# Kernel optimization log

Hardware: AMD Instinct MI355X
Metric: run time of the kernel (lower is better)

## Reference

```python
import jax, jax.numpy as jnp
import numpy as np

N, H = 16, 200
EMB, H1, H2 = 64, 128, 64
NUM_SKILLS = 2000
D_USER, D_ITEM, D_LANG = 100, 100, 10
TIME_BINS = np.array([1, 3600, 24 * 3600, 7 * 24 * 3600], dtype=np.float32)
NUM_TIME_CATS = TIME_BINS.size + 2  # 6

# strictly-lower-triangular pair indices, row-major: pair (i, j) with j < i
PAIR_I, PAIR_J = np.tril_indices(H, k=-1)          # skill_indices, history_indices_selected
P = PAIR_I.size                                    # adjusted_history_len = H*(H-1)/2
ar = np.arange(H)
SUM_IDX = np.concatenate([ar * (ar - 1) // 2, [H * (H - 1) // 2]]).astype(np.int64)  # len H+1


def setup_inputs() -> dict:
    key = jax.random.key(0)
    ks = jax.random.split(key, 16)
    users = jax.random.normal(ks[0], (N, D_USER), jnp.float32)
    items = jax.random.normal(ks[1], (N * H, D_ITEM), jnp.float32)
    langs = jax.random.normal(ks[2], (N * H, D_LANG), jnp.float32)
    skills = jax.random.randint(ks[3], (N, H), 0, NUM_SKILLS)
    timestamps = jnp.sort(jax.random.uniform(ks[4], (N, H), jnp.float32) * 2e6, axis=1)
    targets = (jax.random.uniform(ks[5], (N, H)) > 0.5).astype(jnp.float32)
    mask = jnp.ones((N * H,), dtype=bool)
    emb_table = jax.random.normal(ks[6], (NUM_SKILLS, EMB), jnp.float32) * 0.1
    emb_table = emb_table.at[0].set(0.0)  # padding_idx=0
    W1 = jax.random.normal(ks[7], (H1, 2 * EMB + NUM_TIME_CATS), jnp.float32) * 0.05
    b1 = jnp.zeros((H1,), jnp.float32)
    W2 = jax.random.normal(ks[8], (H2, H1), jnp.float32) * 0.05
    b2 = jnp.zeros((H2,), jnp.float32)
    W3 = jax.random.normal(ks[9], (1, H2), jnp.float32) * 0.05
    b3 = jnp.zeros((1,), jnp.float32)
    num_features = D_USER + D_ITEM + D_LANG + NUM_SKILLS
    linW = jax.random.normal(ks[10], (1, num_features + 2 * NUM_SKILLS), jnp.float32) * 0.01
    linb = jnp.zeros((1,), jnp.float32)
    return {"users": users, "items": items, "langs": langs, "skills": skills,
            "timestamps": timestamps, "targets": targets, "mask": mask,
            "emb_table": emb_table, "W1": W1, "b1": b1, "W2": W2, "b2": b2,
            "W3": W3, "b3": b3, "linW": linW, "linb": linb}


def _forward(users, items, langs, skills, timestamps, targets, mask,
             emb_table, W1, b1, W2, b2, W3, b3, linW, linb):
    bins = jnp.asarray(TIME_BINS)
    pi = jnp.asarray(PAIR_I)
    pj = jnp.asarray(PAIR_J)
    # gather pair embeddings: [N*P, EMB]
    emb = emb_table[skills]                       # [N, H, EMB]
    e_i = emb[:, pi].reshape(-1, EMB)             # skill at position i
    e_j = emb[:, pj].reshape(-1, EMB)             # history skill j < i
    # time-delta categories
    dt = (timestamps[:, pi] - timestamps[:, pj]).reshape(-1)
    cats = jnp.sum(dt[:, None] > bins[None, :], axis=1) + 1
    pad = skills == 0
    pad_pair = pad[:, pi].reshape(-1) | pad[:, pj].reshape(-1)
    cats = jnp.where(pad_pair, 0, cats)
    dt_oh = jax.nn.one_hot(cats, NUM_TIME_CATS, dtype=jnp.float32)
    # pairwise similarity MLP -> tanh scalar, [N, P]
    x = jnp.concatenate([e_i, e_j, dt_oh], axis=1)
    h = jax.nn.relu(x @ W1.T + b1)
    h = jax.nn.relu(h @ W2.T + b2)
    sim = jnp.tanh(h @ W3.T + b3).reshape(N, P)

    sum_idx = jnp.asarray(SUM_IDX)

    def seg_sum(v):  # cumsum-based segment sum over pairs grouped by i -> [N, H]
        cs = jnp.concatenate([jnp.zeros((N, 1), v.dtype), jnp.cumsum(v, axis=1)], axis=1)
        return cs[:, sum_idx[1:]] - cs[:, sum_idx[:-1]]

    flat_skills = skills.reshape(-1)              # [N*H]
    padf = (flat_skills != 0).astype(jnp.float32)
    rows = jnp.arange(N * H)
    v_total = seg_sum(sim).reshape(-1) * padf
    v_correct = seg_sum(sim * targets[:, pi]).reshape(-1) * padf
    tcf = jnp.zeros((N * H, 2 * NUM_SKILLS), jnp.float32)
    tcf = tcf.at[rows, flat_skills].set(v_total)
    tcf = tcf.at[rows, flat_skills + NUM_SKILLS].set(v_correct)

    feats = jnp.concatenate([
        jnp.repeat(users, H, axis=0), items, langs,
        jax.nn.one_hot(flat_skills, NUM_SKILLS, dtype=jnp.float32), tcf], axis=1)
    logits = feats @ linW.T + linb                # [N*H, 1]
    preds = logits.reshape(-1)
    labels = targets.reshape(-1)
    maskf = mask.astype(jnp.float32)
    # BCEWithLogits (reduction='none') + z-term, z_weight=0.0; mask applied as weight
    bce = jnp.logaddexp(0.0, preds) - preds * labels
    eps = 1e-6
    yc = jnp.clip(labels, eps, 1.0 - eps)
    z = jnp.log(yc / (1.0 - yc))
    z_weight = 0.0
    loss = (bce + z_weight * jnp.square(z - preds)) * maskf
    return loss, jax.nn.sigmoid(preds), labels


def reference(users, items, langs, skills, timestamps, targets, mask,
              emb_table, W1, b1, W2, b2, W3, b3, linW, linb):
    return _forward(users, items, langs, skills, timestamps, targets, mask,
                    emb_table, W1, b1, W2, b2, W3, b3, linW, linb)
```

## Files before the change

### kernel.cpp

```cpp
#include <hip/hip_runtime.h>
#include <math.h>

#define N_B     16
#define H_LEN   200
#define NH      3200
#define P_PAIRS 19900
#define NP_TOT  318400
#define EMB     64
#define HID1    128
#define HID2    64
#define NCAT    6
#define W1_COLS 134

#define WS_A    0
#define WS_B    409600
#define WS_C    819200
#define WS_VT   819968
#define WS_W2   823168
#define WS_W1T  827264

#define TI 16
#define NTILE_I 13
#define NTRI (NTILE_I * (NTILE_I + 1) / 2)

typedef __attribute__((ext_vector_type(8))) __bf16 bf16x8;
typedef __attribute__((ext_vector_type(8))) short short8;
typedef __attribute__((ext_vector_type(4))) float f32x4;

__global__ void k0_setup(const float* __restrict__ W1,
                         const float* __restrict__ b1,
                         const float* __restrict__ W2,
                         float* __restrict__ ws) {
    int idx = blockIdx.x * 256 + threadIdx.x;
    if (idx < 17152) {
        int c = idx >> 7, t = idx & 127;
        ws[WS_W1T + c * 128 + t] = W1[t * W1_COLS + c];
        return;
    }
    idx -= 17152;
    if (idx < HID2 * HID1) {
        __bf16 h = (__bf16)W2[idx];
        ((unsigned short*)(ws + WS_W2))[idx] = __builtin_bit_cast(unsigned short, h);
        return;
    }
    idx -= HID2 * HID1;
    if (idx < NCAT * HID1) {
        int c = idx >> 7, t = idx & 127;
        ws[WS_C + idx] = W1[t * W1_COLS + 2 * EMB + c] + b1[t];
        return;
    }
    idx -= NCAT * HID1;
    if (idx < NH) ws[WS_VT + idx] = 0.f;
}

__global__ __launch_bounds__(256)
void k1_ab(const int* __restrict__ skills,
           const float* __restrict__ emb,
           float* __restrict__ ws) {
    __shared__ float e[16][68];
    int t = threadIdx.x;
    int r0 = blockIdx.x * 16;
    {
        int r = t >> 4, c = t & 15;
        int s = skills[r0 + r];
        float4 x = *(const float4*)(emb + (size_t)s * EMB + c * 4);
        *(float4*)&e[r][c * 4] = x;
    }
    __syncthreads();
    int half = t >> 7;
    int c = t & 127;
    const float* w1t = ws + WS_W1T + half * EMB * 128;
    float acc[16];
    #pragma unroll
    for (int r = 0; r < 16; ++r) acc[r] = 0.f;
    #pragma unroll 4
    for (int k0 = 0; k0 < EMB; k0 += 4) {
        float wv0 = w1t[(k0 + 0) * 128 + c];
        float wv1 = w1t[(k0 + 1) * 128 + c];
        float wv2 = w1t[(k0 + 2) * 128 + c];
        float wv3 = w1t[(k0 + 3) * 128 + c];
        #pragma unroll
        for (int r = 0; r < 16; ++r) {
            float4 ev = *(const float4*)&e[r][k0];
            acc[r] = fmaf(wv0, ev.x, acc[r]);
            acc[r] = fmaf(wv1, ev.y, acc[r]);
            acc[r] = fmaf(wv2, ev.z, acc[r]);
            acc[r] = fmaf(wv3, ev.w, acc[r]);
        }
    }
    size_t outbase = half ? WS_B : WS_A;
    #pragma unroll
    for (int r = 0; r < 16; ++r)
        ws[outbase + (size_t)(r0 + r) * HID1 + c] = acc[r];
}

__global__ __launch_bounds__(256, 2)
void k2_mfma(const int* __restrict__ skills,
             const float* __restrict__ ts,
             const float* __restrict__ b2,
             const float* __restrict__ W3,
             const float* __restrict__ b3,
             float* __restrict__ ws) {
    __shared__ float Asm[TI][132];
    __shared__ float Bsm[TI][132];
    __shared__ float Csm[NCAT][132];
    __shared__ float tsi[TI], tsj[TI];
    __shared__ int   ski[TI], skj[TI];

    int t = threadIdx.x, lane = t & 63, w = t >> 6;
    int col = lane & 15, quad = lane >> 4;

    int bid = blockIdx.x;
    int n = bid & 15;
    int tt = bid >> 4;
    int ti = (int)((sqrtf(8.f * (float)tt + 1.f) - 1.f) * 0.5f);
    while (ti * (ti + 1) / 2 > tt) --ti;
    while ((ti + 1) * (ti + 2) / 2 <= tt) ++ti;
    int tj = tt - ti * (ti + 1) / 2;
    int i0 = ti * TI, j0 = tj * TI;
    int base = n * H_LEN;
    bool diag = (ti == tj);

    const short8* w2p = (const short8*)(ws + WS_W2);
    short8 afr[4][4];
    #pragma unroll
    for (int mt = 0; mt < 4; ++mt)
        #pragma unroll
        for (int kk = 0; kk < 4; ++kk)
            afr[mt][kk] = w2p[(mt * 16 + col) * 16 + kk * 4 + quad];
    float b2v[16], w3v[16];
    #pragma unroll
    for (int mt = 0; mt < 4; ++mt)
        #pragma unroll
        for (int r = 0; r < 4; ++r) {
            int u = mt * 16 + quad * 4 + r;
            b2v[mt * 4 + r] = b2[u];
            w3v[mt * 4 + r] = W3[u];
        }
    float b3s = b3[0];

    {
        int r = t >> 5, c = t & 31;
        int gi = min(i0 + r, H_LEN - 1);
        int gi2 = min(i0 + r + 8, H_LEN - 1);
        *(float4*)&Asm[r][c * 4]     = *(const float4*)(ws + WS_A + (size_t)(base + gi)  * HID1 + c * 4);
        *(float4*)&Asm[r + 8][c * 4] = *(const float4*)(ws + WS_A + (size_t)(base + gi2) * HID1 + c * 4);
        int gj = min(j0 + r, H_LEN - 1);
        int gj2 = min(j0 + r + 8, H_LEN - 1);
        *(float4*)&Bsm[r][c * 4]     = *(const float4*)(ws + WS_B + (size_t)(base + gj)  * HID1 + c * 4);
        *(float4*)&Bsm[r + 8][c * 4] = *(const float4*)(ws + WS_B + (size_t)(base + gj2) * HID1 + c * 4);
        if (t < NCAT * 32) {
            int cr = t >> 5, cc = t & 31;
            *(float4*)&Csm[cr][cc * 4] = *(const float4*)(ws + WS_C + cr * HID1 + cc * 4);
        }
        if (t < TI) {
            int gii = min(i0 + t, H_LEN - 1);
            int gjj = min(j0 + t, H_LEN - 1);
            tsi[t] = ts[base + gii]; ski[t] = skills[base + gii];
            tsj[t] = ts[base + gjj]; skj[t] = skills[base + gjj];
        }
    }
    __syncthreads();

    #pragma unroll
    for (int s = 0; s < 4; ++s) {
        int ii = w * 4 + s;
        int gi = i0 + ii;
        if (gi >= H_LEN) continue;
        if (diag && ii == 0) continue;

        int si = ski[ii];  float tsiv = tsi[ii];
        int sj = skj[col]; float tsjv = tsj[col];
        float dtv = tsiv - tsjv;
        int cat = (si == 0 || sj == 0) ? 0
                : 1 + (dtv > 1.f) + (dtv > 3600.f) + (dtv > 86400.f) + (dtv > 604800.f);

        f32x4 acc[4] = {{0.f, 0.f, 0.f, 0.f}, {0.f, 0.f, 0.f, 0.f},
                        {0.f, 0.f, 0.f, 0.f}, {0.f, 0.f, 0.f, 0.f}};
        #pragma unroll
        for (int kk = 0; kk < 4; ++kk) {
            int d0 = kk * 32 + quad * 8;
            float4 a0 = *(const float4*)&Asm[ii][d0];
            float4 a1 = *(const float4*)&Asm[ii][d0 + 4];
            float4 bb0 = *(const float4*)&Bsm[col][d0];
            float4 bb1 = *(const float4*)&Bsm[col][d0 + 4];
            float4 c0 = *(const float4*)&Csm[cat][d0];
            float4 c1 = *(const float4*)&Csm[cat][d0 + 4];
            bf16x8 v;
            v[0] = (__bf16)fmaxf(a0.x + bb0.x + c0.x, 0.f);
            v[1] = (__bf16)fmaxf(a0.y + bb0.y + c0.y, 0.f);
            v[2] = (__bf16)fmaxf(a0.z + bb0.z + c0.z, 0.f);
            v[3] = (__bf16)fmaxf(a0.w + bb0.w + c0.w, 0.f);
            v[4] = (__bf16)fmaxf(a1.x + bb1.x + c1.x, 0.f);
            v[5] = (__bf16)fmaxf(a1.y + bb1.y + c1.y, 0.f);
            v[6] = (__bf16)fmaxf(a1.z + bb1.z + c1.z, 0.f);
            v[7] = (__bf16)fmaxf(a1.w + bb1.w + c1.w, 0.f);
            #pragma unroll
            for (int mt = 0; mt < 4; ++mt)
                acc[mt] = __builtin_amdgcn_mfma_f32_16x16x32_bf16(
                    __builtin_bit_cast(bf16x8, afr[mt][kk]), v, acc[mt], 0, 0, 0);
        }

        float partial = 0.f;
        #pragma unroll
        for (int mt = 0; mt < 4; ++mt)
            #pragma unroll
            for (int r = 0; r < 4; ++r) {
                float h2 = fmaxf(acc[mt][r] + b2v[mt * 4 + r], 0.f);
                partial = fmaf(h2, w3v[mt * 4 + r], partial);
            }
        partial += __shfl_xor(partial, 16);
        partial += __shfl_xor(partial, 32);
        float sim = tanhf(partial + b3s);

        int gj = j0 + col;
        bool valid = (gj < gi);
        sim = valid ? sim : 0.f;
        sim += __shfl_xor(sim, 1);
        sim += __shfl_xor(sim, 2);
        sim += __shfl_xor(sim, 4);
        sim += __shfl_xor(sim, 8);
        if (lane == 0) atomicAdd(&ws[WS_VT + base + gi], sim);
    }
}

__global__ __launch_bounds__(256)
void k3_final(const float* __restrict__ users,
              const float* __restrict__ items,
              const float* __restrict__ langs,
              const int* __restrict__ skills,
              const float* __restrict__ targets,
              const float* __restrict__ linW,
              const float* __restrict__ linb,
              const float* __restrict__ ws,
              float* __restrict__ out) {
    int r = blockIdx.x * 4 + (threadIdx.x >> 6);
    int lane = threadIdx.x & 63;
    int n = r / H_LEN;
    float acc = 0.f;
    for (int idx = lane; idx < 210; idx += 64) {
        float f;
        if (idx < 100)      f = users[n * 100 + idx];
        else if (idx < 200) f = items[r * 100 + (idx - 100)];
        else                f = langs[r * 10 + (idx - 200)];
        acc = fmaf(f, linW[idx], acc);
    }
    #pragma unroll
    for (int off = 32; off > 0; off >>= 1) acc += __shfl_xor(acc, off);
    if (lane == 0) {
        int s = skills[r];
        float tgt = targets[r];
        float vtv = ws[WS_VT + r];
        if (s == 0) vtv = 0.f;
        float vcv = vtv * tgt;
        float logit = acc + linW[210 + s] + vtv * linW[2210 + s]
                    + vcv * linW[4210 + s] + linb[0];
        float sp = logit > 0.f ? logit + log1pf(expf(-logit)) : log1pf(expf(logit));
        float loss = sp - logit * tgt;
        float sig = 1.f / (1.f + expf(-logit));
        out[r]          = loss;
        out[NH + r]     = sig;
        out[2 * NH + r] = tgt;
    }
}

extern "C" void kernel_launch(void* const* d_in, const int* in_sizes, int n_in,
                              void* d_out, int out_size, void* d_ws, size_t ws_size,
                              hipStream_t stream) {
    const float* users   = (const float*)d_in[0];
    const float* items   = (const float*)d_in[1];
    const float* langs   = (const float*)d_in[2];
    const int*   skills  = (const int*)d_in[3];
    const float* ts      = (const float*)d_in[4];
    const float* targets = (const float*)d_in[5];
    const float* emb     = (const float*)d_in[7];
    const float* W1      = (const float*)d_in[8];
    const float* b1      = (const float*)d_in[9];
    const float* W2      = (const float*)d_in[10];
    const float* b2      = (const float*)d_in[11];
    const float* W3      = (const float*)d_in[12];
    const float* b3      = (const float*)d_in[13];
    const float* linW    = (const float*)d_in[14];
    const float* linb    = (const float*)d_in[15];
    float* ws  = (float*)d_ws;
    float* out = (float*)d_out;

    hipLaunchKernelGGL(k0_setup, dim3(115), dim3(256), 0, stream, W1, b1, W2, ws);
    hipLaunchKernelGGL(k1_ab, dim3(NH / 16), dim3(256), 0, stream, skills, emb, ws);
    hipLaunchKernelGGL(k2_mfma, dim3(N_B * NTRI), dim3(256), 0, stream,
                       skills, ts, b2, W3, b3, ws);
    hipLaunchKernelGGL(k3_final, dim3(NH / 4), dim3(256), 0, stream,
                       users, items, langs, skills, targets, linW, linb, ws, out);
}
```

Measured before the change: 125.0 us.

## Store hidden-layer projections in bf16 and pre-swizzle W2 fragments

The per-row A/B projections and the category+bias table are now stored as bf16 instead of fp32. This halves workspace traffic and LDS footprint, and the first-layer sum is unpacked with bit shifts. W2 is pre-permuted into MFMA fragment order so each lane makes one coalesced load. The B row is hoisted out of the per-i loop, occupancy is raised to 3 waves via launch bounds, and tanhf is replaced with a clamped exp-based formula. The cost is extra rounding of the layer-1 partial sums to bf16 before the add and ReLU.

```diff
diff --git a/kernel.cpp b/kernel.cpp
--- a/kernel.cpp
+++ b/kernel.cpp
@@ -4,28 +4,41 @@
 #define N_B     16
 #define H_LEN   200
 #define NH      3200
-#define P_PAIRS 19900
-#define NP_TOT  318400
 #define EMB     64
 #define HID1    128
 #define HID2    64
 #define NCAT    6
 #define W1_COLS 134
 
-#define WS_A    0
-#define WS_B    409600
-#define WS_C    819200
-#define WS_VT   819968
-#define WS_W2   823168
-#define WS_W1T  827264
-
 #define TI 16
 #define NTILE_I 13
 #define NTRI (NTILE_I * (NTILE_I + 1) / 2)
 
+#define WS_VT   0
+#define WS_W2F  3200
+#define WS_CB   7296
+#define WS_W1T  7680
+#define WS_A    24832
+#define WS_B    229632
+
 typedef __attribute__((ext_vector_type(8))) __bf16 bf16x8;
-typedef __attribute__((ext_vector_type(8))) short short8;
+typedef __attribute__((ext_vector_type(8))) unsigned short ushort8;
 typedef __attribute__((ext_vector_type(4))) float f32x4;
+
+__device__ __forceinline__ unsigned short bfbits(float x) {
+    return __builtin_bit_cast(unsigned short, (__bf16)x);
+}
+__device__ __forceinline__ void h1two(unsigned a, unsigned b, unsigned c,
+                                      bf16x8& v, int p) {
+    float s0 = __builtin_bit_cast(float, a << 16)
+             + __builtin_bit_cast(float, b << 16)
+             + __builtin_bit_cast(float, c << 16);
+    float s1 = __builtin_bit_cast(float, a & 0xFFFF0000u)
+             + __builtin_bit_cast(float, b & 0xFFFF0000u)
+             + __builtin_bit_cast(float, c & 0xFFFF0000u);
+    v[p]     = (__bf16)fmaxf(s0, 0.f);
+    v[p + 1] = (__bf16)fmaxf(s1, 0.f);
+}
 
 __global__ void k0_setup(const float* __restrict__ W1,
                          const float* __restrict__ b1,
@@ -38,15 +51,17 @@
         return;
     }
     idx -= 17152;
-    if (idx < HID2 * HID1) {
-        __bf16 h = (__bf16)W2[idx];
-        ((unsigned short*)(ws + WS_W2))[idx] = __builtin_bit_cast(unsigned short, h);
+    if (idx < 8192) {
+        int e = idx & 7, lane = (idx >> 3) & 63, f = idx >> 9;
+        int mt = f >> 2, kk = f & 3, col = lane & 15, quad = lane >> 4;
+        float w = W2[(mt * 16 + col) * HID1 + (kk * 4 + quad) * 8 + e];
+        ((unsigned short*)(ws + WS_W2F))[idx] = bfbits(w);
         return;
     }
-    idx -= HID2 * HID1;
+    idx -= 8192;
     if (idx < NCAT * HID1) {
         int c = idx >> 7, t = idx & 127;
-        ws[WS_C + idx] = W1[t * W1_COLS + 2 * EMB + c] + b1[t];
+        ((unsigned short*)(ws + WS_CB))[idx] = bfbits(W1[t * W1_COLS + 2 * EMB + c] + b1[t]);
         return;
     }
     idx -= NCAT * HID1;
@@ -88,22 +103,22 @@
             acc[r] = fmaf(wv3, ev.w, acc[r]);
         }
     }
-    size_t outbase = half ? WS_B : WS_A;
+    unsigned short* dst = (unsigned short*)(ws + (half ? WS_B : WS_A));
     #pragma unroll
     for (int r = 0; r < 16; ++r)
-        ws[outbase + (size_t)(r0 + r) * HID1 + c] = acc[r];
-}
-
-__global__ __launch_bounds__(256, 2)
+        dst[(size_t)(r0 + r) * HID1 + c] = bfbits(acc[r]);
+}
+
+__global__ __launch_bounds__(256, 3)
 void k2_mfma(const int* __restrict__ skills,
              const float* __restrict__ ts,
              const float* __restrict__ b2,
              const float* __restrict__ W3,
              const float* __restrict__ b3,
              float* __restrict__ ws) {
-    __shared__ float Asm[TI][132];
-    __shared__ float Bsm[TI][132];
-    __shared__ float Csm[NCAT][132];
+    __shared__ unsigned short Asm[TI][136];
+    __shared__ unsigned short Bsm[TI][136];
+    __shared__ unsigned short Csm[NCAT][136];
     __shared__ float tsi[TI], tsj[TI];
     __shared__ int   ski[TI], skj[TI];
 
@@ -121,13 +136,13 @@
     int base = n * H_LEN;
     bool diag = (ti == tj);
 
-    const short8* w2p = (const short8*)(ws + WS_W2);
-    short8 afr[4][4];
+    const ushort8* w2f = (const ushort8*)(ws + WS_W2F);
+    bf16x8 afr[4][4];
     #pragma unroll
     for (int mt = 0; mt < 4; ++mt)
         #pragma unroll
         for (int kk = 0; kk < 4; ++kk)
-            afr[mt][kk] = w2p[(mt * 16 + col) * 16 + kk * 4 + quad];
+            afr[mt][kk] = __builtin_bit_cast(bf16x8, w2f[(mt * 4 + kk) * 64 + lane]);
     float b2v[16], w3v[16];
     #pragma unroll
     for (int mt = 0; mt < 4; ++mt)
@@ -140,18 +155,17 @@
     float b3s = b3[0];
 
     {
-        int r = t >> 5, c = t & 31;
+        int r = t >> 4, c = t & 15;
         int gi = min(i0 + r, H_LEN - 1);
-        int gi2 = min(i0 + r + 8, H_LEN - 1);
-        *(float4*)&Asm[r][c * 4]     = *(const float4*)(ws + WS_A + (size_t)(base + gi)  * HID1 + c * 4);
-        *(float4*)&Asm[r + 8][c * 4] = *(const float4*)(ws + WS_A + (size_t)(base + gi2) * HID1 + c * 4);
         int gj = min(j0 + r, H_LEN - 1);
-        int gj2 = min(j0 + r + 8, H_LEN - 1);
-        *(float4*)&Bsm[r][c * 4]     = *(const float4*)(ws + WS_B + (size_t)(base + gj)  * HID1 + c * 4);
-        *(float4*)&Bsm[r + 8][c * 4] = *(const float4*)(ws + WS_B + (size_t)(base + gj2) * HID1 + c * 4);
-        if (t < NCAT * 32) {
-            int cr = t >> 5, cc = t & 31;
-            *(float4*)&Csm[cr][cc * 4] = *(const float4*)(ws + WS_C + cr * HID1 + cc * 4);
+        const unsigned short* pA = (const unsigned short*)(ws + WS_A);
+        const unsigned short* pB = (const unsigned short*)(ws + WS_B);
+        *(ushort8*)&Asm[r][c * 8] = *(const ushort8*)(pA + (size_t)(base + gi) * HID1 + c * 8);
+        *(ushort8*)&Bsm[r][c * 8] = *(const ushort8*)(pB + (size_t)(base + gj) * HID1 + c * 8);
+        if (t < NCAT * 16) {
+            int cr = t >> 4, cc = t & 15;
+            *(ushort8*)&Csm[cr][cc * 8] =
+                *(const ushort8*)((const unsigned short*)(ws + WS_CB) + cr * HID1 + cc * 8);
         }
         if (t < TI) {
             int gii = min(i0 + t, H_LEN - 1);
@@ -162,6 +176,12 @@
     }
     __syncthreads();
 
+    uint4 braw[4];
+    #pragma unroll
+    for (int kk = 0; kk < 4; ++kk)
+        braw[kk] = *(const uint4*)&Bsm[col][kk * 32 + quad * 8];
+    int sj = skj[col]; float tsjv = tsj[col];
+
     #pragma unroll
     for (int s = 0; s < 4; ++s) {
         int ii = w * 4 + s;
@@ -170,7 +190,6 @@
         if (diag && ii == 0) continue;
 
         int si = ski[ii];  float tsiv = tsi[ii];
-        int sj = skj[col]; float tsjv = tsj[col];
         float dtv = tsiv - tsjv;
         int cat = (si == 0 || sj == 0) ? 0
                 : 1 + (dtv > 1.f) + (dtv > 3600.f) + (dtv > 86400.f) + (dtv > 604800.f);
@@ -179,26 +198,18 @@
                         {0.f, 0.f, 0.f, 0.f}, {0.f, 0.f, 0.f, 0.f}};
         #pragma unroll
         for (int kk = 0; kk < 4; ++kk) {
-            int d0 = kk * 32 + quad * 8;
-            float4 a0 = *(const float4*)&Asm[ii][d0];
-            float4 a1 = *(const float4*)&Asm[ii][d0 + 4];
-            float4 bb0 = *(const float4*)&Bsm[col][d0];
-            float4 bb1 = *(const float4*)&Bsm[col][d0 + 4];
-            float4 c0 = *(const float4*)&Csm[cat][d0];
-            float4 c1 = *(const float4*)&Csm[cat][d0 + 4];
+            uint4 au = *(const uint4*)&Asm[ii][kk * 32 + quad * 8];
+            uint4 cu = *(const uint4*)&Csm[cat][kk * 32 + quad * 8];
+            uint4 bu = braw[kk];
             bf16x8 v;
-            v[0] = (__bf16)fmaxf(a0.x + bb0.x + c0.x, 0.f);
-            v[1] = (__bf16)fmaxf(a0.y + bb0.y + c0.y, 0.f);
-            v[2] = (__bf16)fmaxf(a0.z + bb0.z + c0.z, 0.f);
-            v[3] = (__bf16)fmaxf(a0.w + bb0.w + c0.w, 0.f);
-            v[4] = (__bf16)fmaxf(a1.x + bb1.x + c1.x, 0.f);
-            v[5] = (__bf16)fmaxf(a1.y + bb1.y + c1.y, 0.f);
-            v[6] = (__bf16)fmaxf(a1.z + bb1.z + c1.z, 0.f);
-            v[7] = (__bf16)fmaxf(a1.w + bb1.w + c1.w, 0.f);
+            h1two(au.x, bu.x, cu.x, v, 0);
+            h1two(au.y, bu.y, cu.y, v, 2);
+            h1two(au.z, bu.z, cu.z, v, 4);
+            h1two(au.w, bu.w, cu.w, v, 6);
             #pragma unroll
             for (int mt = 0; mt < 4; ++mt)
                 acc[mt] = __builtin_amdgcn_mfma_f32_16x16x32_bf16(
-                    __builtin_bit_cast(bf16x8, afr[mt][kk]), v, acc[mt], 0, 0, 0);
+                    afr[mt][kk], v, acc[mt], 0, 0, 0);
         }
 
         float partial = 0.f;
@@ -211,7 +222,9 @@
             }
         partial += __shfl_xor(partial, 16);
         partial += __shfl_xor(partial, 32);
-        float sim = tanhf(partial + b3s);
+        float xc = fminf(fmaxf(partial + b3s, -15.f), 15.f);
+        float e2 = __expf(2.f * xc);
+        float sim = (e2 - 1.f) / (e2 + 1.f);
 
         int gj = j0 + col;
         bool valid = (gj < gi);
```

Result: faster. 119.9 us (-4.1%).
